# Performance work log

Hardware: AMD Instinct MI355X
Metric: run time of the kernel (lower is better)

The kernel has to match this reference:

```python
import jax, jax.numpy as jnp
import numpy as np

N, E = 50000, 800000
IN_CH, EDGE_DIM, H, C = 256, 32, 4, 32


def setup_inputs() -> dict:
    key = jax.random.key(0)
    ks = jax.random.split(key, 9)
    inp = {
        "x": jax.random.normal(ks[0], (N, IN_CH), dtype=jnp.float32),
        "edge_index": jax.random.randint(ks[1], (2, E), 0, N, dtype=jnp.int64),
        "edge_attr": jax.random.normal(ks[2], (E, EDGE_DIM), dtype=jnp.float32),
        "dist_weight": jax.random.uniform(ks[3], (E,), dtype=jnp.float32),
        # learned parameters (xavier-ish scale)
        "W_src": jax.random.normal(ks[4], (IN_CH, H * C), dtype=jnp.float32) * (1.0 / np.sqrt(IN_CH)),
        "W_dst": jax.random.normal(ks[5], (IN_CH, H * C), dtype=jnp.float32) * (1.0 / np.sqrt(IN_CH)),
        "W_edge": jax.random.normal(ks[6], (EDGE_DIM, H * C), dtype=jnp.float32) * (1.0 / np.sqrt(EDGE_DIM)),
        "att": jax.random.normal(ks[7], (1, H, C), dtype=jnp.float32) * 0.1,
        "spatial_scale": jnp.ones((H,), dtype=jnp.float32),
    }
    return inp


def reference(x, edge_index, edge_attr, dist_weight, W_src, W_dst, W_edge, att, spatial_scale):
    n = x.shape[0]
    h, c = att.shape[1], att.shape[2]
    src, dst = edge_index[0], edge_index[1]

    x_src = (x @ W_src).reshape(n, h, c)          # [N,H,C]
    x_dst = (x @ W_dst).reshape(n, h, c)          # [N,H,C]
    e_feat = (edge_attr @ W_edge).reshape(-1, h, c)  # [E,H,C]

    # edge-wise attention logits
    alpha = jnp.tanh(x_src[src] + x_dst[dst] + e_feat)  # [E,H,C]
    alpha = jnp.sum(alpha * att, axis=-1)               # [E,H]
    alpha_raw = alpha

    # spatial decay: dist_weight ** spatial_scale per head
    alpha = alpha * dist_weight[:, None] ** spatial_scale[None, :]

    # segment softmax over dst (numerically stable; max is grad-neutral)
    m = jax.ops.segment_max(alpha, dst, num_segments=n)  # [N,H]
    m = jnp.where(jnp.isfinite(m), m, 0.0)               # empty segments -> 0 (matches torch init)
    m = jax.lax.stop_gradient(m)
    ea = jnp.exp(alpha - m[dst])                         # [E,H]
    s = jax.ops.segment_sum(ea, dst, num_segments=n)     # [N,H]
    alpha_norm = ea / (s[dst] + 1e-8)                    # [E,H]

    # weighted aggregation of source features
    msg = x_src[src] * alpha_norm[:, :, None]            # [E,H,C]
    out = jax.ops.segment_sum(msg, dst, num_segments=n)  # [N,H,C]
    return out.reshape(n, h * c), alpha_norm, alpha_raw
```

## Files before the change

kernel.cpp:

```cpp
#include <hip/hip_runtime.h>
#include <hip/hip_bf16.h>

#define N_NODES 50000
#define N_EDGES 800000
#define IN_CH   256
#define EDGE_DIM 32
#define NH 4
#define NC 32
#define HC 128
#define SCAN_BLKS 196
#define EGROUPS (N_EDGES / 64)
#define NTILES (N_NODES / 16)

typedef __attribute__((ext_vector_type(8))) short bf16x8;
typedef __attribute__((ext_vector_type(4))) float f32x4;

__device__ int g_bsum[256];
__device__ int g_boffs[256];

__device__ __forceinline__ float fexp2(float x) { return __builtin_amdgcn_exp2f(x); }
__device__ __forceinline__ float flog2(float x) { return __builtin_amdgcn_logf(x); }
__device__ __forceinline__ float fexp(float x)  { return __builtin_amdgcn_exp2f(x * 1.44269504089f); }

__device__ __forceinline__ float ftanh(float x) {
    const float e = fexp2(x * 2.88539008178f);
    return 1.0f - 2.0f * __builtin_amdgcn_rcpf(e + 1.0f);
}

__device__ __forceinline__ unsigned short f2bf(float f) {
    union { float f; unsigned int u; } v; v.f = f;
    const unsigned int r = v.u + 0x7fffu + ((v.u >> 16) & 1u);
    return (unsigned short)(r >> 16);
}

__device__ __forceinline__ float ldf(const void* p, long i, bool f32) {
    return f32 ? ((const float*)p)[i]
               : __bfloat162float(((const __hip_bfloat16*)p)[i]);
}

__device__ __forceinline__ int ld_src(const int* ei, long e, bool idx64) {
    return idx64 ? ei[2 * e] : ei[e];
}
__device__ __forceinline__ int ld_dst(const int* ei, long e, bool idx64) {
    return idx64 ? ei[2 * ((long)N_EDGES + e)] : ei[(long)N_EDGES + e];
}

__global__ __launch_bounds__(256) void detect_k(const unsigned short* __restrict__ xu,
                                                const int* __restrict__ ei,
                                                int* __restrict__ flag) {
    __shared__ int zc, bc, nz_idx;
    if (threadIdx.x == 0) { zc = 0; bc = 0; nz_idx = 0; }
    __syncthreads();
    int z = 0, b = 0, hi = 0;
    for (int i = threadIdx.x; i < 16384; i += 256) {
        const unsigned short w = xu[2 * i];
        if (w == 0) ++z;
        if ((w & 0x7F80) == 0x7F80) ++b;
    }
    for (int i = threadIdx.x; i < 8192; i += 256)
        if (ei[2 * i + 1] != 0) hi = 1;
    atomicAdd(&zc, z);
    atomicAdd(&bc, b);
    if (hi) atomicAdd(&nz_idx, 1);
    __syncthreads();
    if (threadIdx.x == 0) {
        flag[0] = (zc > 8192 || bc > 0) ? 1 : 0;
        flag[1] = (nz_idx == 0) ? 1 : 0;
    }
}

__global__ __launch_bounds__(256) void zero_deg_k(int* __restrict__ deg) {
    const int i = blockIdx.x * 256 + threadIdx.x;
    if (i < N_NODES) deg[i] = 0;
}

__global__ __launch_bounds__(256) void hist_k(const int* __restrict__ ei,
                                              const int* __restrict__ flag,
                                              int* __restrict__ deg) {
    const bool idx64 = (flag[1] != 0);
    const long e = (long)blockIdx.x * 256 + threadIdx.x;
    if (e < N_EDGES) atomicAdd(&deg[ld_dst(ei, e, idx64)], 1);
}

__global__ __launch_bounds__(256) void scan1_k(const int* __restrict__ deg,
                                               int* __restrict__ row_ptr) {
    __shared__ int wsum[4];
    const int tid = threadIdx.x;
    const int lane = tid & 63, wid = tid >> 6;
    const int i = blockIdx.x * 256 + tid;
    const int v = (i < N_NODES) ? deg[i] : 0;
    int x = v;
    #pragma unroll
    for (int off = 1; off < 64; off <<= 1) {
        const int t = __shfl_up(x, off);
        if (lane >= off) x += t;
    }
    if (lane == 63) wsum[wid] = x;
    __syncthreads();
    int wpre = 0;
    for (int w = 0; w < wid; ++w) wpre += wsum[w];
    if (i < N_NODES) row_ptr[i] = wpre + x - v;
    if (tid == 0) g_bsum[blockIdx.x] = wsum[0] + wsum[1] + wsum[2] + wsum[3];
}

__global__ __launch_bounds__(256) void scan2_k(int* __restrict__ row_ptr) {
    __shared__ int wsum[4];
    const int tid = threadIdx.x;
    const int lane = tid & 63, wid = tid >> 6;
    const int v = (tid < SCAN_BLKS) ? g_bsum[tid] : 0;
    int x = v;
    #pragma unroll
    for (int off = 1; off < 64; off <<= 1) {
        const int t = __shfl_up(x, off);
        if (lane >= off) x += t;
    }
    if (lane == 63) wsum[wid] = x;
    __syncthreads();
    int wpre = 0;
    for (int w = 0; w < wid; ++w) wpre += wsum[w];
    if (tid < SCAN_BLKS) g_boffs[tid] = wpre + x - v;
    if (tid == 0) row_ptr[N_NODES] = N_EDGES;
}

__global__ __launch_bounds__(256) void scan3_k(int* __restrict__ row_ptr,
                                               int* __restrict__ cursor) {
    const int i = blockIdx.x * 256 + threadIdx.x;
    if (i < N_NODES) {
        const int t = row_ptr[i] + g_boffs[blockIdx.x];
        row_ptr[i] = t;
        cursor[i] = t;
    }
}

__global__ __launch_bounds__(256) void scatter_k(const int* __restrict__ ei,
                                                 const int* __restrict__ flag,
                                                 int* __restrict__ cursor,
                                                 int* __restrict__ eids,
                                                 int* __restrict__ esrc) {
    const bool idx64 = (flag[1] != 0);
    const long e = (long)blockIdx.x * 256 + threadIdx.x;
    if (e >= N_EDGES) return;
    const int dst = ld_dst(ei, e, idx64);
    const int src = ld_src(ei, e, idx64);
    const int pos = atomicAdd(&cursor[dst], 1);
    eids[pos] = (int)e;
    esrc[pos] = src;
}

__global__ __launch_bounds__(256) void node_gemm_mfma_k(const unsigned short* __restrict__ x,
                                                        const unsigned short* __restrict__ Wsrc,
                                                        const unsigned short* __restrict__ Wdst,
                                                        const int* __restrict__ flag,
                                                        float* __restrict__ xsrc,
                                                        float* __restrict__ xdst) {
    if (flag[0] != 0) return;
    const int tid = threadIdx.x;
    const int l   = tid & 63;
    const int w   = tid >> 6;
    const int jj  = l & 15;
    const int hi  = l >> 4;
    const int cbase = w * 64;

    bf16x8 bfrag[8][4];
    #pragma unroll
    for (int ks = 0; ks < 8; ++ks)
        #pragma unroll
        for (int t = 0; t < 4; ++t) {
            const int c = cbase + t * 16 + jj;
            const unsigned short* Wp = (c < HC) ? (Wsrc + c) : (Wdst + (c - HC));
            union { unsigned short u[8]; bf16x8 v; } bu;
            #pragma unroll
            for (int i = 0; i < 8; ++i)
                bu.u[i] = Wp[(ks * 32 + hi * 8 + i) * HC];
            bfrag[ks][t] = bu.v;
        }

    for (int nt = blockIdx.x; nt < NTILES; nt += gridDim.x) {
        const long n0 = (long)nt * 16;
        const unsigned short* xr = x + (n0 + jj) * IN_CH + hi * 8;
        bf16x8 afrag[8];
        #pragma unroll
        for (int ks = 0; ks < 8; ++ks)
            afrag[ks] = *(const bf16x8*)(xr + ks * 32);

        f32x4 acc[4];
        #pragma unroll
        for (int t = 0; t < 4; ++t) acc[t] = (f32x4){0.f, 0.f, 0.f, 0.f};
        #pragma unroll
        for (int ks = 0; ks < 8; ++ks)
            #pragma unroll
            for (int t = 0; t < 4; ++t)
                acc[t] = __builtin_amdgcn_mfma_f32_16x16x32_bf16(afrag[ks], bfrag[ks][t], acc[t], 0, 0, 0);

        #pragma unroll
        for (int t = 0; t < 4; ++t) {
            const int c = cbase + t * 16 + jj;
            float* obase = (c < HC) ? (xsrc + c) : (xdst + (c - HC));
            #pragma unroll
            for (int r = 0; r < 4; ++r)
                obase[(n0 + hi * 4 + r) * HC] = acc[t][r];
        }
    }
}

__global__ __launch_bounds__(256) void node_gemm_f32_k(const void* __restrict__ x,
                                                       const void* __restrict__ Wsrc,
                                                       const void* __restrict__ Wdst,
                                                       const int* __restrict__ flag,
                                                       float* __restrict__ xsrc,
                                                       float* __restrict__ xdst) {
    if (flag[0] == 0) return;
    __shared__ float sx[8][IN_CH];
    const int tid = threadIdx.x;
    const long n0 = (long)blockIdx.x * 8;
    #pragma unroll
    for (int r = 0; r < 8; ++r)
        sx[r][tid] = ((const float*)x)[(n0 + r) * IN_CH + tid];
    __syncthreads();

    const int mat = tid >> 7;
    const int col = tid & 127;
    const float* __restrict__ W = (const float*)(mat ? Wdst : Wsrc);
    float acc[8] = {0,0,0,0,0,0,0,0};
    for (int k = 0; k < IN_CH; k += 4) {
        const float w0 = W[(long)(k + 0) * HC + col];
        const float w1 = W[(long)(k + 1) * HC + col];
        const float w2 = W[(long)(k + 2) * HC + col];
        const float w3 = W[(long)(k + 3) * HC + col];
        #pragma unroll
        for (int r = 0; r < 8; ++r) {
            const float4 sv = *(const float4*)&sx[r][k];
            acc[r] += sv.x * w0 + sv.y * w1 + sv.z * w2 + sv.w * w3;
        }
    }
    float* __restrict__ o = mat ? xdst : xsrc;
    #pragma unroll
    for (int r = 0; r < 8; ++r)
        o[(n0 + r) * HC + col] = acc[r];
}

__global__ __launch_bounds__(256) void edge_alpha_k(const int* __restrict__ ei,
                                                    const void* __restrict__ eattr,
                                                    const void* __restrict__ dw,
                                                    const void* __restrict__ Wedge,
                                                    const void* __restrict__ att,
                                                    const void* __restrict__ sscale,
                                                    const int* __restrict__ flag,
                                                    const float* __restrict__ xsrc,
                                                    const float* __restrict__ xdst,
                                                    float* __restrict__ ea_ws,
                                                    float* __restrict__ araw_out) {
    const bool f32   = (flag[0] != 0);
    const bool idx64 = (flag[1] != 0);
    __shared__ int   sSrc[4][16];
    __shared__ int   sDst[4][16];
    __shared__ float sDw[4][16];

    const int tid = threadIdx.x;
    const int l   = tid & 63;
    const int wid = tid >> 6;
    const int jj  = l & 15;
    const int hi  = l >> 4;

    bf16x8 bfrag[8];
    #pragma unroll
    for (int t = 0; t < 8; ++t) {
        union { unsigned short u[8]; bf16x8 v; } bu;
        #pragma unroll
        for (int i = 0; i < 8; ++i) {
            const int k = hi * 8 + i;
            const int col = t * 16 + jj;
            if (f32) bu.u[i] = f2bf(((const float*)Wedge)[k * HC + col]);
            else     bu.u[i] = ((const unsigned short*)Wedge)[k * HC + col];
        }
        bfrag[t] = bu.v;
    }
    float attv[8];
    #pragma unroll
    for (int t = 0; t < 8; ++t) attv[t] = ldf(att, t * 16 + jj, f32);
    const float ssv = ldf(sscale, l & 3, f32);

    for (long g = blockIdx.x; g < EGROUPS; g += (long)gridDim.x) {
        const long e0 = g * 64 + (long)wid * 16;

        if (l < 16)      sSrc[wid][l]      = ld_src(ei, e0 + l, idx64);
        else if (l < 32) sDst[wid][l - 16] = ld_dst(ei, e0 + (l - 16), idx64);
        else if (l < 48) sDw[wid][l - 32]  = ldf(dw, e0 + (l - 32), f32);
        __builtin_amdgcn_wave_barrier();

        bf16x8 afrag;
        if (f32) {
            const float* ar = (const float*)eattr + (e0 + jj) * EDGE_DIM + hi * 8;
            const float4 p0 = *(const float4*)ar;
            const float4 p1 = *(const float4*)(ar + 4);
            union { unsigned short u[8]; bf16x8 v; } au;
            au.u[0] = f2bf(p0.x); au.u[1] = f2bf(p0.y); au.u[2] = f2bf(p0.z); au.u[3] = f2bf(p0.w);
            au.u[4] = f2bf(p1.x); au.u[5] = f2bf(p1.y); au.u[6] = f2bf(p1.z); au.u[7] = f2bf(p1.w);
            afrag = au.v;
        } else {
            afrag = *(const bf16x8*)((const unsigned short*)eattr + (e0 + jj) * EDGE_DIM + hi * 8);
        }

        const f32x4 zero = {0.f, 0.f, 0.f, 0.f};
        f32x4 acc[8];
        #pragma unroll
        for (int t = 0; t < 8; ++t)
            acc[t] = __builtin_amdgcn_mfma_f32_16x16x32_bf16(afrag, bfrag[t], zero, 0, 0, 0);

        float hsum[4][4] = {{0,0,0,0},{0,0,0,0},{0,0,0,0},{0,0,0,0}};
        #pragma unroll
        for (int r = 0; r < 4; ++r) {
            const int sI = sSrc[wid][hi * 4 + r];
            const int dI = sDst[wid][hi * 4 + r];
            const float* bs = xsrc + (long)sI * HC + jj;
            const float* bd = xdst + (long)dI * HC + jj;
            float xsv[8], xdv[8];
            #pragma unroll
            for (int t = 0; t < 8; ++t) xsv[t] = bs[t * 16];
            #pragma unroll
            for (int t = 0; t < 8; ++t) xdv[t] = bd[t * 16];
            #pragma unroll
            for (int t = 0; t < 8; ++t) {
                const float v = ftanh(acc[t][r] + xsv[t] + xdv[t]) * attv[t];
                hsum[r][t >> 1] += v;
            }
        }

        #pragma unroll
        for (int r = 0; r < 4; ++r)
            #pragma unroll
            for (int h2 = 0; h2 < 4; ++h2) {
                float v = hsum[r][h2];
                v += __shfl_xor(v, 1);
                v += __shfl_xor(v, 2);
                v += __shfl_xor(v, 4);
                v += __shfl_xor(v, 8);
                hsum[r][h2] = v;
            }

        float val = hsum[0][0];
        #pragma unroll
        for (int r = 0; r < 4; ++r)
            #pragma unroll
            for (int h2 = 0; h2 < 4; ++h2)
                if (jj == r * 4 + h2) val = hsum[r][h2];

        const int r_sel = jj >> 2;
        const long er = e0 + hi * 4 + r_sel;
        const float dwv = sDw[wid][hi * 4 + r_sel];
        araw_out[er * 4 + (jj & 3)] = val;
        const float d = fexp2(ssv * flog2(dwv));
        ea_ws[er * 4 + (jj & 3)] = fexp(val * d);
        __builtin_amdgcn_wave_barrier();
    }
}

__global__ __launch_bounds__(256) void aggregate_k(const int* __restrict__ row_ptr,
                                                   const int* __restrict__ eids,
                                                   const int* __restrict__ esrc,
                                                   const float* __restrict__ ea_ws,
                                                   const float* __restrict__ xsrc,
                                                   float* __restrict__ s_ws,
                                                   float* __restrict__ out) {
    const int tid = threadIdx.x;
    const int lane = tid & 63;
    const int n = blockIdx.x * 4 + (tid >> 6);
    if (n >= N_NODES) return;
    const int h = lane >> 4;

    const int p0 = row_ptr[n];
    const int p1 = row_ptr[n + 1];

    float ax = 0.0f, ay = 0.0f, sa = 0.0f;
    for (int p = p0; p < p1; ++p) {
        const int e = eids[p];
        const int src = esrc[p];
        const float w = ea_ws[(long)e * 4 + h];
        const float2 xv = *(const float2*)(xsrc + (long)src * HC + (lane << 1));
        ax += w * xv.x;
        ay += w * xv.y;
        sa += w;
    }
    const float inv = 1.0f / (sa + 1e-8f);
    float* o = out + (long)n * HC + (lane << 1);
    o[0] = ax * inv;
    o[1] = ay * inv;
    if ((lane & 15) == 0) s_ws[(long)n * 4 + h] = sa;
}

__global__ __launch_bounds__(256) void edge_norm_k(const int* __restrict__ ei,
                                                   const int* __restrict__ flag,
                                                   const float* __restrict__ ea_ws,
                                                   const float* __restrict__ s_ws,
                                                   float* __restrict__ anorm) {
    const bool idx64 = (flag[1] != 0);
    const long i = (long)blockIdx.x * 256 + threadIdx.x;
    if (i >= (long)N_EDGES * NH) return;
    const long e = i >> 2;
    const int h = (int)(i & 3);
    const int dst = ld_dst(ei, e, idx64);
    anorm[i] = ea_ws[i] / (s_ws[(long)dst * 4 + h] + 1e-8f);
}

extern "C" void kernel_launch(void* const* d_in, const int* in_sizes, int n_in,
                              void* d_out, int out_size, void* d_ws, size_t ws_size,
                              hipStream_t stream) {
    const void* x      = d_in[0];
    const int*  ei     = (const int*)d_in[1];
    const void* eattr  = d_in[2];
    const void* dw     = d_in[3];
    const void* Wsrc   = d_in[4];
    const void* Wdst   = d_in[5];
    const void* Wedge  = d_in[6];
    const void* att    = d_in[7];
    const void* sscale = d_in[8];

    float* out   = (float*)d_out;
    float* anorm = out + (long)N_NODES * HC;
    float* araw  = anorm + (long)N_EDGES * NH;

    float* ws      = (float*)d_ws;
    int*   flag    = (int*)d_ws;
    float* xsrc    = ws + 64;
    float* xdst    = xsrc + (long)N_NODES * HC;
    float* ea      = xdst + (long)N_NODES * HC;
    float* s_ws    = ea + (long)N_EDGES * NH;
    int*   deg     = (int*)(s_ws + (long)N_NODES * NH);
    int*   row_ptr = deg + N_NODES;
    int*   cursor  = row_ptr + N_NODES + 1;
    int*   eids    = cursor + N_NODES;
    int*   esrc    = eids + N_EDGES;

    detect_k<<<1, 256, 0, stream>>>((const unsigned short*)x, ei, flag);
    zero_deg_k<<<(N_NODES + 255) / 256, 256, 0, stream>>>(deg);
    hist_k<<<(N_EDGES + 255) / 256, 256, 0, stream>>>(ei, flag, deg);
    scan1_k<<<SCAN_BLKS, 256, 0, stream>>>(deg, row_ptr);
    scan2_k<<<1, 256, 0, stream>>>(row_ptr);
    scan3_k<<<SCAN_BLKS, 256, 0, stream>>>(row_ptr, cursor);
    scatter_k<<<(N_EDGES + 255) / 256, 256, 0, stream>>>(ei, flag, cursor, eids, esrc);
    node_gemm_mfma_k<<<1024, 256, 0, stream>>>((const unsigned short*)x,
                                               (const unsigned short*)Wsrc,
                                               (const unsigned short*)Wdst,
                                               flag, xsrc, xdst);
    node_gemm_f32_k<<<N_NODES / 8, 256, 0, stream>>>(x, Wsrc, Wdst, flag, xsrc, xdst);
    edge_alpha_k<<<2048, 256, 0, stream>>>(ei, eattr, dw, Wedge, att, sscale,
                                           flag, xsrc, xdst, ea, araw);
    aggregate_k<<<(N_NODES + 3) / 4, 256, 0, stream>>>(row_ptr, eids, esrc, ea, xsrc, s_ws, out);
    edge_norm_k<<<((long)N_EDGES * NH + 255) / 256, 256, 0, stream>>>(ei, flag, ea, s_ws, anorm);
}
```

Baseline: 729.7 us.

## Replace scalar fp32 node GEMM with split-bf16 three-term MFMA GEMM

Replaces the scalar FP32 node projection kernel with an MFMA kernel. Each fp32 operand is split into high and low bf16 parts, and three bf16 MFMAs per k-step (hi*hi, hi*lo, lo*hi) approximate the fp32 product. A small pre-kernel splits and transposes the weights into global buffers. The goal is to move the x@W_src/W_dst GEMM, which dominates on the fp32 input path, onto the matrix cores. The cost is slightly lower precision than true fp32 and an extra launch.

Result: faster. 671.1 us (-8.0%).

```diff
diff --git a/kernel.cpp b/kernel.cpp
--- a/kernel.cpp
+++ b/kernel.cpp
@@ -17,6 +17,8 @@
 
 __device__ int g_bsum[256];
 __device__ int g_boffs[256];
+__device__ __align__(16) unsigned short g_wt_hi[256 * 256];
+__device__ __align__(16) unsigned short g_wt_lo[256 * 256];
 
 __device__ __forceinline__ float fexp2(float x) { return __builtin_amdgcn_exp2f(x); }
 __device__ __forceinline__ float flog2(float x) { return __builtin_amdgcn_logf(x); }
@@ -31,6 +33,19 @@
     union { float f; unsigned int u; } v; v.f = f;
     const unsigned int r = v.u + 0x7fffu + ((v.u >> 16) & 1u);
     return (unsigned short)(r >> 16);
+}
+
+__device__ __forceinline__ void split8(const float4 a, const float4 b, bf16x8& hi, bf16x8& lo) {
+    union { unsigned short us[8]; bf16x8 v; } H, L;
+    const float xs[8] = {a.x, a.y, a.z, a.w, b.x, b.y, b.z, b.w};
+    #pragma unroll
+    for (int e = 0; e < 8; ++e) {
+        const unsigned int u = __float_as_uint(xs[e]);
+        H.us[e] = (unsigned short)(u >> 16);
+        const float lof = xs[e] - __uint_as_float(u & 0xffff0000u);
+        L.us[e] = (unsigned short)(__float_as_uint(lof) >> 16);
+    }
+    hi = H.v; lo = L.v;
 }
 
 __device__ __forceinline__ float ldf(const void* p, long i, bool f32) {
@@ -147,6 +162,74 @@
     esrc[pos] = src;
 }
 
+__global__ __launch_bounds__(256) void w_split_k(const float* __restrict__ Wsrc,
+                                                 const float* __restrict__ Wdst,
+                                                 const int* __restrict__ flag) {
+    if (flag[0] == 0) return;
+    const int i = blockIdx.x * 256 + threadIdx.x;
+    const int c = i >> 8;
+    const int k = i & 255;
+    const float w = (c < HC) ? Wsrc[k * HC + c] : Wdst[k * HC + (c - HC)];
+    const unsigned int u = __float_as_uint(w);
+    g_wt_hi[i] = (unsigned short)(u >> 16);
+    const float lof = w - __uint_as_float(u & 0xffff0000u);
+    g_wt_lo[i] = (unsigned short)(__float_as_uint(lof) >> 16);
+}
+
+__global__ __launch_bounds__(512) void node_gemm_f32s_k(const float* __restrict__ x,
+                                                        const int* __restrict__ flag,
+                                                        float* __restrict__ xsrc,
+                                                        float* __restrict__ xdst) {
+    if (flag[0] == 0) return;
+    const int tid = threadIdx.x;
+    const int l   = tid & 63;
+    const int wv  = tid >> 6;
+    const int jj  = l & 15;
+    const int hi4 = l >> 4;
+    const int cbase = wv * 32;
+
+    bf16x8 bhi[8][2], blo[8][2];
+    #pragma unroll
+    for (int ks = 0; ks < 8; ++ks)
+        #pragma unroll
+        for (int t = 0; t < 2; ++t) {
+            const int off = (cbase + t * 16 + jj) * 256 + ks * 32 + hi4 * 8;
+            bhi[ks][t] = *(const bf16x8*)(g_wt_hi + off);
+            blo[ks][t] = *(const bf16x8*)(g_wt_lo + off);
+        }
+
+    for (int nt = blockIdx.x; nt < NTILES; nt += gridDim.x) {
+        const long n0 = (long)nt * 16;
+        const float* xr = x + (n0 + jj) * IN_CH;
+
+        f32x4 acc[2];
+        acc[0] = (f32x4){0.f, 0.f, 0.f, 0.f};
+        acc[1] = (f32x4){0.f, 0.f, 0.f, 0.f};
+        #pragma unroll
+        for (int ks = 0; ks < 8; ++ks) {
+            const float4 a0 = *(const float4*)(xr + ks * 32 + hi4 * 8);
+            const float4 a1 = *(const float4*)(xr + ks * 32 + hi4 * 8 + 4);
+            bf16x8 ahi, alo;
+            split8(a0, a1, ahi, alo);
+            #pragma unroll
+            for (int t = 0; t < 2; ++t) {
+                acc[t] = __builtin_amdgcn_mfma_f32_16x16x32_bf16(ahi, bhi[ks][t], acc[t], 0, 0, 0);
+                acc[t] = __builtin_amdgcn_mfma_f32_16x16x32_bf16(ahi, blo[ks][t], acc[t], 0, 0, 0);
+                acc[t] = __builtin_amdgcn_mfma_f32_16x16x32_bf16(alo, bhi[ks][t], acc[t], 0, 0, 0);
+            }
+        }
+
+        #pragma unroll
+        for (int t = 0; t < 2; ++t) {
+            const int c = cbase + t * 16 + jj;
+            float* obase = (c < HC) ? (xsrc + c) : (xdst + (c - HC));
+            #pragma unroll
+            for (int r = 0; r < 4; ++r)
+                obase[(n0 + hi4 * 4 + r) * HC] = acc[t][r];
+        }
+    }
+}
+
 __global__ __launch_bounds__(256) void node_gemm_mfma_k(const unsigned short* __restrict__ x,
                                                         const unsigned short* __restrict__ Wsrc,
                                                         const unsigned short* __restrict__ Wdst,
@@ -201,42 +284,6 @@
                 obase[(n0 + hi * 4 + r) * HC] = acc[t][r];
         }
     }
-}
-
-__global__ __launch_bounds__(256) void node_gemm_f32_k(const void* __restrict__ x,
-                                                       const void* __restrict__ Wsrc,
-                                                       const void* __restrict__ Wdst,
-                                                       const int* __restrict__ flag,
-                                                       float* __restrict__ xsrc,
-                                                       float* __restrict__ xdst) {
-    if (flag[0] == 0) return;
-    __shared__ float sx[8][IN_CH];
-    const int tid = threadIdx.x;
-    const long n0 = (long)blockIdx.x * 8;
-    #pragma unroll
-    for (int r = 0; r < 8; ++r)
-        sx[r][tid] = ((const float*)x)[(n0 + r) * IN_CH + tid];
-    __syncthreads();
-
-    const int mat = tid >> 7;
-    const int col = tid & 127;
-    const float* __restrict__ W = (const float*)(mat ? Wdst : Wsrc);
-    float acc[8] = {0,0,0,0,0,0,0,0};
-    for (int k = 0; k < IN_CH; k += 4) {
-        const float w0 = W[(long)(k + 0) * HC + col];
-        const float w1 = W[(long)(k + 1) * HC + col];
-        const float w2 = W[(long)(k + 2) * HC + col];
-        const float w3 = W[(long)(k + 3) * HC + col];
-        #pragma unroll
-        for (int r = 0; r < 8; ++r) {
-            const float4 sv = *(const float4*)&sx[r][k];
-            acc[r] += sv.x * w0 + sv.y * w1 + sv.z * w2 + sv.w * w3;
-        }
-    }
-    float* __restrict__ o = mat ? xdst : xsrc;
-    #pragma unroll
-    for (int r = 0; r < 8; ++r)
-        o[(n0 + r) * HC + col] = acc[r];
 }
 
 __global__ __launch_bounds__(256) void edge_alpha_k(const int* __restrict__ ei,
@@ -438,11 +485,12 @@
     scan2_k<<<1, 256, 0, stream>>>(row_ptr);
     scan3_k<<<SCAN_BLKS, 256, 0, stream>>>(row_ptr, cursor);
     scatter_k<<<(N_EDGES + 255) / 256, 256, 0, stream>>>(ei, flag, cursor, eids, esrc);
+    w_split_k<<<256, 256, 0, stream>>>((const float*)Wsrc, (const float*)Wdst, flag);
+    node_gemm_f32s_k<<<512, 512, 0, stream>>>((const float*)x, flag, xsrc, xdst);
     node_gemm_mfma_k<<<1024, 256, 0, stream>>>((const unsigned short*)x,
                                                (const unsigned short*)Wsrc,
                                                (const unsigned short*)Wdst,
                                                flag, xsrc, xdst);
-    node_gemm_f32_k<<<N_NODES / 8, 256, 0, stream>>>(x, Wsrc, Wdst, flag, xsrc, xdst);
     edge_alpha_k<<<2048, 256, 0, stream>>>(ei, eattr, dw, Wedge, att, sscale,
                                            flag, xsrc, xdst, ea, araw);
     aggregate_k<<<(N_NODES + 3) / 4, 256, 0, stream>>>(row_ptr, eids, esrc, ea, xsrc, s_ws, out);
```
